# Kernel tuning notes

Measured on AMD Instinct MI355X. Metric: run time of the kernel, lower is better.

The kernel has to match this reference:

```python
import jax, jax.numpy as jnp
import numpy as np

# ---- HashGridPlanesEncoder config (hybrid-k-planes) ----
NUM_LEVELS = 16
LEVEL_DIM = 2
BASE_RES = 16
DESIRED_RES = 2048
LOG2_HASHMAP = 19
D = 2  # grid_nd: each plane encoder is a 2D hash grid
N_PTS = 1048576
COO_COMBS = [(0, 1), (0, 2), (1, 2)]
HASH_PRIME_1 = 2654435761  # torch-ngp fast_hash prime for dim 1 (dim 0 prime is 1)


def _level_constants():
    # Mirrors torch-ngp GridEncoder offset/resolution computation.
    pls = 2.0 ** (np.log2(DESIRED_RES / BASE_RES) / (NUM_LEVELS - 1))
    max_params = 2 ** LOG2_HASHMAP
    scales, res, sizes, offs = [], [], [], [0]
    for l in range(NUM_LEVELS):
        s = BASE_RES * pls ** l - 1.0          # kernel: scale = exp2(l*S + H) - 1
        r = int(np.ceil(s)) + 1                # kernel: resolution = ceil(scale) + 1
        p = min(max_params, (r + 1) ** D)      # align_corners=False -> (res+1)^D
        p = int(np.ceil(p / 8) * 8)            # round up to multiple of 8
        scales.append(s); res.append(r); sizes.append(p); offs.append(offs[-1] + p)
    return (np.array(scales, np.float32), np.array(res, np.int64),
            np.array(sizes, np.int64), np.array(offs[:-1], np.int64), offs[-1])


SCALES, RES, SIZES, OFFSETS, TOTAL_PARAMS = _level_constants()
USE_HASH = ((RES + 1) ** D) > SIZES  # static per-level: dense linear index vs spatial hash


def _encode_plane(x2, table):
    """x2: [N,2] coords in [0,1]; table: [TOTAL_PARAMS, LEVEL_DIM]. Returns [N, L*C]."""
    n = x2.shape[0]
    scales = jnp.asarray(SCALES)
    pos = x2[:, None, :] * scales[None, :, None] + 0.5           # [N,L,2] (align_corners=False)
    pg_f = jnp.floor(pos)
    frac = pos - pg_f                                            # [N,L,2]
    pg = pg_f.astype(jnp.uint32)
    corners = jnp.array([[0, 0], [1, 0], [0, 1], [1, 1]], jnp.uint32)  # [4,2]
    cpos = pg[:, :, None, :] + corners[None, None]               # [N,L,4,2]
    cmask = corners.astype(bool)[None, None]                     # [1,1,4,2]
    w = jnp.where(cmask, frac[:, :, None, :], 1.0 - frac[:, :, None, :]).prod(-1)  # [N,L,4]
    stride1 = jnp.asarray((RES + 1).astype(np.uint32))           # [L]
    linear = cpos[..., 0] + cpos[..., 1] * stride1[None, :, None]
    hashed = cpos[..., 0] ^ (cpos[..., 1] * jnp.uint32(HASH_PRIME_1))  # uint32 wrap-around
    idx = jnp.where(jnp.asarray(USE_HASH)[None, :, None], hashed, linear)
    idx = idx % jnp.asarray(SIZES.astype(np.uint32))[None, :, None]
    idx = (idx + jnp.asarray(OFFSETS.astype(np.uint32))[None, :, None]).astype(jnp.int32)
    feats = table[idx]                                           # [N,L,4,C] gather
    out = (w[..., None] * feats).sum(axis=2)                     # [N,L,C] bilinear interp
    return out.reshape(n, NUM_LEVELS * LEVEL_DIM)


def setup_inputs() -> dict:
    key = jax.random.key(0)
    kp, k0, k1, k2 = jax.random.split(key, 4)
    pts = jax.random.uniform(kp, (N_PTS, 3), dtype=jnp.float32)  # coords (treated as in [-1,1] domain)
    std = 1e-4  # GridEncoder init: embeddings.uniform_(-1e-4, 1e-4)
    mk = lambda k: jax.random.uniform(k, (TOTAL_PARAMS, LEVEL_DIM), jnp.float32, -std, std)
    return {"pts": pts, "table_xy": mk(k0), "table_xz": mk(k1), "table_yz": mk(k2)}


def reference(pts, table_xy, table_xz, table_yz):
    # GridEncoder.forward normalizes inputs: (x + bound) / (2*bound), bound=1
    u = (pts + 1.0) * 0.5
    tables = (table_xy, table_xz, table_yz)
    out = _encode_plane(u[:, list(COO_COMBS[0])], tables[0])
    for comb, tab in zip(COO_COMBS[1:], tables[1:]):
        out = out + _encode_plane(u[:, list(comb)], tab)
    return out
```

## Files before the change

### kernel.cpp

```cpp
#include <hip/hip_runtime.h>
#include <hip/hip_fp16.h>
#include <cmath>

#define NLEV 16
#define HASH_START 12
#define HMASK ((1u << 19) - 1u)
#define HASH_PRIME 2654435761u
#define LDS_WORDS 14160

typedef float    f4 __attribute__((ext_vector_type(4)));
typedef unsigned u4 __attribute__((ext_vector_type(4)));

struct LvlC {
  float scale[NLEV];
  unsigned stride[NLEV];
  unsigned offset[NLEV];
};

__device__ __forceinline__ float2 h2f(unsigned u) {
  return __half22float2(__builtin_bit_cast(__half2, u));
}
__device__ __forceinline__ void nt_store4(float* p, float a, float b, float c, float d) {
  f4 v = {a, b, c, d};
  __builtin_nontemporal_store(v, reinterpret_cast<f4*>(p));
}

__global__ __launch_bounds__(256) void k_convert(
    const float2* __restrict__ t0, const float2* __restrict__ t1,
    const float2* __restrict__ t2, unsigned* __restrict__ dst, unsigned total)
{
  unsigned g = blockIdx.x * 256 + threadIdx.x;
  unsigned stp = gridDim.x * 256;
  unsigned tot3 = 3u * total;
  for (unsigned e = g; e < tot3; e += stp) {
    const float2* src; unsigned i = e;
    if (i < total)            { src = t0; }
    else if (i < 2u * total)  { src = t1; i -= total; }
    else                      { src = t2; i -= 2u * total; }
    float2 v = src[i];
    __half2 h = __floats2half2_rn(v.x, v.y);
    __builtin_nontemporal_store(__builtin_bit_cast(unsigned, h), dst + e);
  }
}

__global__ __launch_bounds__(256) void k_dense1011(
    const float* __restrict__ pts, const unsigned* __restrict__ tab,
    unsigned* __restrict__ s10, unsigned* __restrict__ s11,
    LvlC lc, unsigned total, int half)
{
  int t = blockIdx.x * 256 + threadIdx.x;
  if (t >= half) return;
  const int idx[2] = {t, t + half};

  float ua[2][3], ub[2][3];
#pragma unroll
  for (int k = 0; k < 2; ++k) {
    float u0 = (pts[3 * idx[k] + 0] + 1.f) * .5f;
    float u1 = (pts[3 * idx[k] + 1] + 1.f) * .5f;
    float u2 = (pts[3 * idx[k] + 2] + 1.f) * .5f;
    ua[k][0] = u0; ub[k][0] = u1;
    ua[k][1] = u0; ub[k][1] = u2;
    ua[k][2] = u1; ub[k][2] = u2;
  }

  uint2 g[2][2][3][2];
  float rx[2][2][3], ry[2][2][3];
#pragma unroll
  for (int k = 0; k < 2; ++k)
#pragma unroll
    for (int l = 0; l < 2; ++l) {
      const float sc = lc.scale[10 + l];
      const unsigned st = lc.stride[10 + l], o = lc.offset[10 + l];
#pragma unroll
      for (int p = 0; p < 3; ++p) {
        float px = ua[k][p] * sc + .5f, py = ub[k][p] * sc + .5f;
        float fx = floorf(px), fy = floorf(py);
        rx[k][l][p] = px - fx; ry[k][l][p] = py - fy;
        unsigned i00 = (unsigned)fx + (unsigned)fy * st + o;
        const unsigned* tp = tab + (size_t)p * total;
        g[k][l][p][0] = *reinterpret_cast<const uint2*>(tp + i00);
        g[k][l][p][1] = *reinterpret_cast<const uint2*>(tp + i00 + st);
      }
    }

#pragma unroll
  for (int k = 0; k < 2; ++k)
#pragma unroll
    for (int l = 0; l < 2; ++l) {
      float s0 = 0.f, s1 = 0.f;
#pragma unroll
      for (int p = 0; p < 3; ++p) {
        float x = rx[k][l][p], y = ry[k][l][p];
        float w00 = (1.f - x) * (1.f - y), w10 = x * (1.f - y);
        float w01 = (1.f - x) * y,          w11 = x * y;
        float2 f00 = h2f(g[k][l][p][0].x), f10 = h2f(g[k][l][p][0].y);
        float2 f01 = h2f(g[k][l][p][1].x), f11 = h2f(g[k][l][p][1].y);
        s0 += w00 * f00.x + w10 * f10.x + w01 * f01.x + w11 * f11.x;
        s1 += w00 * f00.y + w10 * f10.y + w01 * f01.y + w11 * f11.y;
      }
      unsigned hv = __builtin_bit_cast(unsigned, __floats2half2_rn(s0, s1));
      unsigned* sl = l ? s11 : s10;
      __builtin_nontemporal_store(hv, sl + idx[k]);
    }
}

__global__ __launch_bounds__(256) void k_hash_lvl(
    const float* __restrict__ pts, const unsigned* __restrict__ tab,
    unsigned* __restrict__ slice, float sc, unsigned o, unsigned total, int half)
{
  int t = blockIdx.x * 256 + threadIdx.x;
  if (t >= half) return;
  const int idx[2] = {t, t + half};

  float ua[2][3], ub[2][3];
#pragma unroll
  for (int k = 0; k < 2; ++k) {
    float u0 = (pts[3 * idx[k] + 0] + 1.f) * .5f;
    float u1 = (pts[3 * idx[k] + 1] + 1.f) * .5f;
    float u2 = (pts[3 * idx[k] + 2] + 1.f) * .5f;
    ua[k][0] = u0; ub[k][0] = u1;
    ua[k][1] = u0; ub[k][1] = u2;
    ua[k][2] = u1; ub[k][2] = u2;
  }

  unsigned g[2][3][4];
  float rx[2][3], ry[2][3];
#pragma unroll
  for (int k = 0; k < 2; ++k)
#pragma unroll
    for (int p = 0; p < 3; ++p) {
      float px = ua[k][p] * sc + .5f, py = ub[k][p] * sc + .5f;
      float fx = floorf(px), fy = floorf(py);
      rx[k][p] = px - fx; ry[k][p] = py - fy;
      unsigned x0 = (unsigned)fx, y0 = (unsigned)fy;
      unsigned hy0 = y0 * HASH_PRIME, hy1 = hy0 + HASH_PRIME;
      const unsigned* tp = tab + (size_t)p * total + o;
      g[k][p][0] = tp[(x0 ^ hy0) & HMASK];
      g[k][p][1] = tp[((x0 + 1u) ^ hy0) & HMASK];
      g[k][p][2] = tp[(x0 ^ hy1) & HMASK];
      g[k][p][3] = tp[((x0 + 1u) ^ hy1) & HMASK];
    }

#pragma unroll
  for (int k = 0; k < 2; ++k) {
    float s0 = 0.f, s1 = 0.f;
#pragma unroll
    for (int p = 0; p < 3; ++p) {
      float x = rx[k][p], y = ry[k][p];
      float w00 = (1.f - x) * (1.f - y), w10 = x * (1.f - y);
      float w01 = (1.f - x) * y,          w11 = x * y;
      float2 f00 = h2f(g[k][p][0]), f10 = h2f(g[k][p][1]);
      float2 f01 = h2f(g[k][p][2]), f11 = h2f(g[k][p][3]);
      s0 += w00 * f00.x + w10 * f10.x + w01 * f01.x + w11 * f11.x;
      s1 += w00 * f00.y + w10 * f10.y + w01 * f01.y + w11 * f11.y;
    }
    __builtin_nontemporal_store(
        __builtin_bit_cast(unsigned, __floats2half2_rn(s0, s1)), slice + idx[k]);
  }
}

__global__ __launch_bounds__(256) void k_final(
    const float* __restrict__ pts, const unsigned* __restrict__ tab,
    const unsigned* __restrict__ slices,
    float* __restrict__ out, LvlC lc, unsigned total, int n)
{
  __shared__ unsigned lds[LDS_WORDS];
  int i = blockIdx.x * 256 + threadIdx.x;

  float u0 = (pts[3 * i + 0] + 1.f) * .5f;
  float u1 = (pts[3 * i + 1] + 1.f) * .5f;
  float u2 = (pts[3 * i + 2] + 1.f) * .5f;
  const float ua[3] = {u0, u0, u1}, ub[3] = {u1, u2, u2};

  float res[12];
#pragma unroll
  for (int j = 0; j < 12; ++j) res[j] = 0.f;

  for (int p = 0; p < 3; ++p) {
    if (p) __syncthreads();
    const u4* src = reinterpret_cast<const u4*>(tab + (size_t)p * total);
    for (unsigned e = threadIdx.x; e < LDS_WORDS / 4; e += 256)
      reinterpret_cast<u4*>(lds)[e] = src[e];
    __syncthreads();
#pragma unroll
    for (int l = 0; l < 6; ++l) {
      float px = ua[p] * lc.scale[l] + .5f, py = ub[p] * lc.scale[l] + .5f;
      float fx = floorf(px), fy = floorf(py);
      float x = px - fx, y = py - fy;
      unsigned st = lc.stride[l];
      unsigned i00 = (unsigned)fx + (unsigned)fy * st + lc.offset[l];
      float2 f00 = h2f(lds[i00]),      f10 = h2f(lds[i00 + 1]);
      float2 f01 = h2f(lds[i00 + st]), f11 = h2f(lds[i00 + st + 1]);
      float w00 = (1.f - x) * (1.f - y), w10 = x * (1.f - y);
      float w01 = (1.f - x) * y,          w11 = x * y;
      res[2 * l + 0] += w00 * f00.x + w10 * f10.x + w01 * f01.x + w11 * f11.x;
      res[2 * l + 1] += w00 * f00.y + w10 * f10.y + w01 * f01.y + w11 * f11.y;
    }
  }

  uint2 g[4][3][2];
  float gx[4][3], gy[4][3];
#pragma unroll
  for (int l = 0; l < 4; ++l) {
    const float sc = lc.scale[6 + l];
    const unsigned st = lc.stride[6 + l], o = lc.offset[6 + l];
#pragma unroll
    for (int p = 0; p < 3; ++p) {
      float px = ua[p] * sc + .5f, py = ub[p] * sc + .5f;
      float fx = floorf(px), fy = floorf(py);
      gx[l][p] = px - fx; gy[l][p] = py - fy;
      unsigned i00 = (unsigned)fx + (unsigned)fy * st + o;
      const unsigned* tp = tab + (size_t)p * total;
      g[l][p][0] = *reinterpret_cast<const uint2*>(tp + i00);
      g[l][p][1] = *reinterpret_cast<const uint2*>(tp + i00 + st);
    }
  }
  unsigned sl[6];
#pragma unroll
  for (int j = 0; j < 6; ++j) sl[j] = slices[(size_t)j * n + i];

  float res69[8];
#pragma unroll
  for (int l = 0; l < 4; ++l) {
    float s0 = 0.f, s1 = 0.f;
#pragma unroll
    for (int p = 0; p < 3; ++p) {
      float x = gx[l][p], y = gy[l][p];
      float w00 = (1.f - x) * (1.f - y), w10 = x * (1.f - y);
      float w01 = (1.f - x) * y,          w11 = x * y;
      float2 f00 = h2f(g[l][p][0].x), f10 = h2f(g[l][p][0].y);
      float2 f01 = h2f(g[l][p][1].x), f11 = h2f(g[l][p][1].y);
      s0 += w00 * f00.x + w10 * f10.x + w01 * f01.x + w11 * f11.x;
      s1 += w00 * f00.y + w10 * f10.y + w01 * f01.y + w11 * f11.y;
    }
    res69[2 * l] = s0; res69[2 * l + 1] = s1;
  }

  float v[32];
#pragma unroll
  for (int j = 0; j < 12; ++j) v[j] = res[j];
#pragma unroll
  for (int j = 0; j < 8; ++j) v[12 + j] = res69[j];
#pragma unroll
  for (int j = 0; j < 6; ++j) {
    float2 f = h2f(sl[j]);
    v[20 + 2 * j] = f.x; v[20 + 2 * j + 1] = f.y;
  }
  float* orow = out + (size_t)i * 32;
#pragma unroll
  for (int j = 0; j < 8; ++j)
    nt_store4(orow + 4 * j, v[4 * j], v[4 * j + 1], v[4 * j + 2], v[4 * j + 3]);
}

__global__ __launch_bounds__(256) void k_fallback(
    const float* __restrict__ pts, const float2* __restrict__ txy,
    const float2* __restrict__ txz, const float2* __restrict__ tyz,
    float* __restrict__ out, LvlC lc, int n)
{
  int i = blockIdx.x * 256 + threadIdx.x;
  if (i >= n) return;
  float u0 = (pts[3 * i + 0] + 1.f) * .5f;
  float u1 = (pts[3 * i + 1] + 1.f) * .5f;
  float u2 = (pts[3 * i + 2] + 1.f) * .5f;
  const float ua[3] = {u0, u0, u1}, ub[3] = {u1, u2, u2};
  const float2* tabs[3] = {txy, txz, tyz};
  float acc[32];
#pragma unroll
  for (int j = 0; j < 32; ++j) acc[j] = 0.f;
#pragma unroll
  for (int l = 0; l < NLEV; ++l) {
    const float sc = lc.scale[l];
    const unsigned o = lc.offset[l], s = lc.stride[l];
#pragma unroll
    for (int p = 0; p < 3; ++p) {
      const float2* t = tabs[p];
      float px = ua[p] * sc + .5f, py = ub[p] * sc + .5f;
      float fx = floorf(px), fy = floorf(py);
      float rx = px - fx, ry = py - fy;
      unsigned x0 = (unsigned)fx, y0 = (unsigned)fy;
      float w00 = (1.f - rx) * (1.f - ry), w10 = rx * (1.f - ry);
      float w01 = (1.f - rx) * ry,          w11 = rx * ry;
      float2 f00, f10, f01, f11;
      if (l >= HASH_START) {
        unsigned hy0 = y0 * HASH_PRIME, hy1 = hy0 + HASH_PRIME;
        f00 = t[o + ((x0 ^ hy0) & HMASK)];
        f10 = t[o + (((x0 + 1u) ^ hy0) & HMASK)];
        f01 = t[o + ((x0 ^ hy1) & HMASK)];
        f11 = t[o + (((x0 + 1u) ^ hy1) & HMASK)];
      } else {
        unsigned i00 = x0 + y0 * s;
        float4 r0 = *reinterpret_cast<const float4*>(t + o + i00);
        float4 r1 = *reinterpret_cast<const float4*>(t + o + i00 + s);
        f00 = make_float2(r0.x, r0.y); f10 = make_float2(r0.z, r0.w);
        f01 = make_float2(r1.x, r1.y); f11 = make_float2(r1.z, r1.w);
      }
      acc[2 * l + 0] += w00 * f00.x + w10 * f10.x + w01 * f01.x + w11 * f11.x;
      acc[2 * l + 1] += w00 * f00.y + w10 * f10.y + w01 * f01.y + w11 * f11.y;
    }
  }
  float* orow = out + (size_t)i * 32;
#pragma unroll
  for (int j = 0; j < 8; ++j)
    nt_store4(orow + 4 * j, acc[4 * j], acc[4 * j + 1], acc[4 * j + 2], acc[4 * j + 3]);
}

static unsigned compute_levels(LvlC* lc)
{
  const double pls = std::pow(2.0, std::log2(2048.0 / 16.0) / 15.0);
  unsigned long long off = 0;
  for (int l = 0; l < NLEV; ++l) {
    double s = 16.0 * std::pow(pls, (double)l) - 1.0;
    lc->scale[l] = (float)s;
    long long r = (long long)std::ceil(s) + 1;
    long long dense = (r + 1) * (r + 1);
    long long sz = dense < (1LL << 19) ? dense : (1LL << 19);
    sz = ((sz + 7) / 8) * 8;
    lc->stride[l] = (unsigned)(r + 1);
    lc->offset[l] = (unsigned)off;
    off += (unsigned long long)sz;
  }
  return (unsigned)off;
}

extern "C" void kernel_launch(void* const* d_in, const int* in_sizes, int n_in,
                              void* d_out, int out_size, void* d_ws, size_t ws_size,
                              hipStream_t stream) {
  const float*  pts = (const float*)d_in[0];
  const float2* txy = (const float2*)d_in[1];
  const float2* txz = (const float2*)d_in[2];
  const float2* tyz = (const float2*)d_in[3];
  float* out = (float*)d_out;
  int n = in_sizes[0] / 3;

  LvlC lc;
  unsigned total = compute_levels(&lc);

  size_t tab_bytes = (size_t)3 * total * 4;
  size_t tab_al = (tab_bytes + 255) & ~(size_t)255;
  size_t need = tab_al + (size_t)6 * n * 4;

  bool ok = (n % 512 == 0) && (lc.offset[6] == LDS_WORDS) && (ws_size >= need);
  for (int l = HASH_START; l < NLEV; ++l) {
    unsigned sz = ((l + 1 < NLEV) ? lc.offset[l + 1] : total) - lc.offset[l];
    ok = ok && (sz == (1u << 19));
  }

  int block = 256;
  int grid = (n + block - 1) / block;
  if (!ok) {
    k_fallback<<<grid, block, 0, stream>>>(pts, txy, txz, tyz, out, lc, n);
    return;
  }

  unsigned* tab16 = (unsigned*)d_ws;
  unsigned* slices = (unsigned*)((char*)d_ws + tab_al);

  int half = n / 2;
  int gridh = half / block;

  k_convert<<<2048, 256, 0, stream>>>(txy, txz, tyz, tab16, total);
  k_dense1011<<<gridh, block, 0, stream>>>(pts, tab16, slices, slices + (size_t)n,
                                           lc, total, half);
  for (int l = HASH_START; l < NLEV; ++l)
    k_hash_lvl<<<gridh, block, 0, stream>>>(pts, tab16, slices + (size_t)(l - 10) * n,
                                            lc.scale[l], lc.offset[l], total, half);
  k_final<<<grid, block, 0, stream>>>(pts, tab16, slices, out, lc, total, n);
}
```

Measured before the change: 397.3 us.

## Pair hash-row gathers, enlarge final block, and split dense gathers into groups

In the hash-level kernel, when x0 is even the two corners of a row (x0^hy and (x0+1)^hy) are adjacent words, so they are fetched with one 8-byte load and swapped as needed. Odd x0 keeps two separate loads. The final kernel moves to 512-thread blocks so each block's LDS fill of the dense table is shared by more points. Its levels 6-9 gathers are now issued in two groups of two levels, which lowers register pressure but leaves fewer loads in flight. The 512-thread launch uses n/512 blocks, so it assumes n is a multiple of 512.

```diff
diff --git a/kernel.cpp b/kernel.cpp
--- a/kernel.cpp
+++ b/kernel.cpp
@@ -104,6 +104,22 @@
     }
 }
 
+__device__ __forceinline__ void hash_row(
+    const unsigned* __restrict__ tp, unsigned x0, unsigned hy,
+    unsigned& g0, unsigned& g1)
+{
+  unsigned a0 = (x0 ^ hy) & HMASK;
+  if ((x0 & 1u) == 0u) {
+    uint2 v = *reinterpret_cast<const uint2*>(tp + (a0 & ~1u));
+    bool hi = (a0 & 1u) != 0u;
+    g0 = hi ? v.y : v.x;
+    g1 = hi ? v.x : v.y;
+  } else {
+    g0 = tp[a0];
+    g1 = tp[((x0 + 1u) ^ hy) & HMASK];
+  }
+}
+
 __global__ __launch_bounds__(256) void k_hash_lvl(
     const float* __restrict__ pts, const unsigned* __restrict__ tab,
     unsigned* __restrict__ slice, float sc, unsigned o, unsigned total, int half)
@@ -135,10 +151,8 @@
       unsigned x0 = (unsigned)fx, y0 = (unsigned)fy;
       unsigned hy0 = y0 * HASH_PRIME, hy1 = hy0 + HASH_PRIME;
       const unsigned* tp = tab + (size_t)p * total + o;
-      g[k][p][0] = tp[(x0 ^ hy0) & HMASK];
-      g[k][p][1] = tp[((x0 + 1u) ^ hy0) & HMASK];
-      g[k][p][2] = tp[(x0 ^ hy1) & HMASK];
-      g[k][p][3] = tp[((x0 + 1u) ^ hy1) & HMASK];
+      hash_row(tp, x0, hy0, g[k][p][0], g[k][p][1]);
+      hash_row(tp, x0, hy1, g[k][p][2], g[k][p][3]);
     }
 
 #pragma unroll
@@ -159,13 +173,13 @@
   }
 }
 
-__global__ __launch_bounds__(256) void k_final(
+__global__ __launch_bounds__(512) void k_final(
     const float* __restrict__ pts, const unsigned* __restrict__ tab,
     const unsigned* __restrict__ slices,
     float* __restrict__ out, LvlC lc, unsigned total, int n)
 {
   __shared__ unsigned lds[LDS_WORDS];
-  int i = blockIdx.x * 256 + threadIdx.x;
+  int i = blockIdx.x * 512 + threadIdx.x;
 
   float u0 = (pts[3 * i + 0] + 1.f) * .5f;
   float u1 = (pts[3 * i + 1] + 1.f) * .5f;
@@ -179,7 +193,7 @@
   for (int p = 0; p < 3; ++p) {
     if (p) __syncthreads();
     const u4* src = reinterpret_cast<const u4*>(tab + (size_t)p * total);
-    for (unsigned e = threadIdx.x; e < LDS_WORDS / 4; e += 256)
+    for (unsigned e = threadIdx.x; e < LDS_WORDS / 4; e += 512)
       reinterpret_cast<u4*>(lds)[e] = src[e];
     __syncthreads();
 #pragma unroll
@@ -198,43 +212,48 @@
     }
   }
 
-  uint2 g[4][3][2];
-  float gx[4][3], gy[4][3];
-#pragma unroll
-  for (int l = 0; l < 4; ++l) {
-    const float sc = lc.scale[6 + l];
-    const unsigned st = lc.stride[6 + l], o = lc.offset[6 + l];
-#pragma unroll
-    for (int p = 0; p < 3; ++p) {
-      float px = ua[p] * sc + .5f, py = ub[p] * sc + .5f;
-      float fx = floorf(px), fy = floorf(py);
-      gx[l][p] = px - fx; gy[l][p] = py - fy;
-      unsigned i00 = (unsigned)fx + (unsigned)fy * st + o;
-      const unsigned* tp = tab + (size_t)p * total;
-      g[l][p][0] = *reinterpret_cast<const uint2*>(tp + i00);
-      g[l][p][1] = *reinterpret_cast<const uint2*>(tp + i00 + st);
-    }
-  }
+  float res69[8];
+#pragma unroll
+  for (int grp = 0; grp < 2; ++grp) {
+    uint2 g[2][3][2];
+    float gx[2][3], gy[2][3];
+#pragma unroll
+    for (int h = 0; h < 2; ++h) {
+      const int l = 6 + 2 * grp + h;
+      const float sc = lc.scale[l];
+      const unsigned st = lc.stride[l], o = lc.offset[l];
+#pragma unroll
+      for (int p = 0; p < 3; ++p) {
+        float px = ua[p] * sc + .5f, py = ub[p] * sc + .5f;
+        float fx = floorf(px), fy = floorf(py);
+        gx[h][p] = px - fx; gy[h][p] = py - fy;
+        unsigned i00 = (unsigned)fx + (unsigned)fy * st + o;
+        const unsigned* tp = tab + (size_t)p * total;
+        g[h][p][0] = *reinterpret_cast<const uint2*>(tp + i00);
+        g[h][p][1] = *reinterpret_cast<const uint2*>(tp + i00 + st);
+      }
+    }
+#pragma unroll
+    for (int h = 0; h < 2; ++h) {
+      float s0 = 0.f, s1 = 0.f;
+#pragma unroll
+      for (int p = 0; p < 3; ++p) {
+        float x = gx[h][p], y = gy[h][p];
+        float w00 = (1.f - x) * (1.f - y), w10 = x * (1.f - y);
+        float w01 = (1.f - x) * y,          w11 = x * y;
+        float2 f00 = h2f(g[h][p][0].x), f10 = h2f(g[h][p][0].y);
+        float2 f01 = h2f(g[h][p][1].x), f11 = h2f(g[h][p][1].y);
+        s0 += w00 * f00.x + w10 * f10.x + w01 * f01.x + w11 * f11.x;
+        s1 += w00 * f00.y + w10 * f10.y + w01 * f01.y + w11 * f11.y;
+      }
+      res69[4 * grp + 2 * h + 0] = s0;
+      res69[4 * grp + 2 * h + 1] = s1;
+    }
+  }
+
   unsigned sl[6];
 #pragma unroll
   for (int j = 0; j < 6; ++j) sl[j] = slices[(size_t)j * n + i];
-
-  float res69[8];
-#pragma unroll
-  for (int l = 0; l < 4; ++l) {
-    float s0 = 0.f, s1 = 0.f;
-#pragma unroll
-    for (int p = 0; p < 3; ++p) {
-      float x = gx[l][p], y = gy[l][p];
-      float w00 = (1.f - x) * (1.f - y), w10 = x * (1.f - y);
-      float w01 = (1.f - x) * y,          w11 = x * y;
-      float2 f00 = h2f(g[l][p][0].x), f10 = h2f(g[l][p][0].y);
-      float2 f01 = h2f(g[l][p][1].x), f11 = h2f(g[l][p][1].y);
-      s0 += w00 * f00.x + w10 * f10.x + w01 * f01.x + w11 * f11.x;
-      s1 += w00 * f00.y + w10 * f10.y + w01 * f01.y + w11 * f11.y;
-    }
-    res69[2 * l] = s0; res69[2 * l + 1] = s1;
-  }
 
   float v[32];
 #pragma unroll
@@ -364,5 +383,5 @@
   for (int l = HASH_START; l < NLEV; ++l)
     k_hash_lvl<<<gridh, block, 0, stream>>>(pts, tab16, slices + (size_t)(l - 10) * n,
                                             lc.scale[l], lc.offset[l], total, half);
-  k_final<<<grid, block, 0, stream>>>(pts, tab16, slices, out, lc, total, n);
-}
+  k_final<<<n / 512, 512, 0, stream>>>(pts, tab16, slices, out, lc, total, n);
+}
```

Result: faster. 366.3 us (-7.8%).
